# Optimization experiments

Hardware: AMD Instinct MI355X
Metric: run time of the kernel (lower is better)

Reference implementation:

```python
import jax, jax.numpy as jnp
import numpy as np

N_QUBITS = 4
B = 524288


def ry_mat(theta):
    # theta: scalar or (B,) -> (..., 2, 2) complex64
    c = jnp.cos(theta / 2).astype(jnp.complex64)
    s = jnp.sin(theta / 2).astype(jnp.complex64)
    return jnp.stack([jnp.stack([c, -s], -1), jnp.stack([s, c], -1)], -2)


def rz_mat(theta):
    e = jnp.exp(-0.5j * theta.astype(jnp.complex64))
    z = jnp.zeros_like(e)
    return jnp.stack([jnp.stack([e, z], -1), jnp.stack([z, jnp.conj(e)], -1)], -2)


def apply_shared(state, gate, wire):
    # state: (B, 2,2,2,2); gate: (2,2) shared across batch
    state = jnp.moveaxis(state, 1 + wire, -1)
    state = jnp.einsum('...a,ca->...c', state, gate)
    return jnp.moveaxis(state, -1, 1 + wire)


def apply_batched(state, gate, wire):
    # gate: (B, 2, 2), per-sample angles
    state = jnp.moveaxis(state, 1 + wire, -1)
    state = jnp.einsum('b...a,bca->b...c', state, gate)
    return jnp.moveaxis(state, -1, 1 + wire)


def cnot_01(state):
    # control wire 0 (axis 1), target wire 1 (axis 2): flip target when control=1
    return jnp.concatenate([state[:, :1], jnp.flip(state[:, 1:], axis=2)], axis=1)


def circuit(x, weights):
    # batched 4-qubit state-vector simulation; state shape (B, 2,2,2,2)
    b = x.shape[0]
    state = jnp.zeros((b,) + (2,) * N_QUBITS, jnp.complex64).at[:, 0, 0, 0, 0].set(1.0)
    # data-encoding RY layer (per-sample angles)
    for i in range(N_QUBITS):
        state = apply_batched(state, ry_mat(x[:, i]), i)
    # two repeats of (RZ, RY per wire) + CNOT(0,1); only weights[0,:,0:2] is used (faithful to source)
    for _rep in range(2):
        for i in range(N_QUBITS):
            state = apply_shared(state, rz_mat(weights[0, i, 0]), i)
            state = apply_shared(state, ry_mat(weights[0, i, 1]), i)
        state = cnot_01(state)
    probs = jnp.real(state * jnp.conj(state))  # (B,2,2,2,2)
    zexp = []
    for i in range(N_QUBITS):
        axes = tuple(a for a in range(1, 1 + N_QUBITS) if a != 1 + i)
        marg = probs.sum(axis=axes)  # (B, 2)
        zexp.append(marg[:, 0] - marg[:, 1])
    return jnp.stack(zexp, axis=-1).astype(jnp.float32)  # (B, 4)


def setup_inputs() -> dict:
    key = jax.random.key(0)
    k1, k2, k3, k4 = jax.random.split(key, 4)
    return {
        'x': jax.random.normal(k1, (B, N_QUBITS), dtype=jnp.float32),
        'weights': jax.random.normal(k2, (2, N_QUBITS, 4), dtype=jnp.float32),
        'head_w': jax.random.normal(k3, (2, N_QUBITS), dtype=jnp.float32) * 0.5,
        'head_b': jax.random.normal(k4, (2,), dtype=jnp.float32) * 0.1,
    }


def reference(x, weights, head_w, head_b):
    q = circuit(x, weights)            # (B, 4) PauliZ expectations
    return q @ head_w.T + head_b       # Linear(4, 2)
```

## Files before the change

kernel.cpp:

```cpp
#include <hip/hip_runtime.h>

#define NQ  4
#define DIM 16

__global__ __launch_bounds__(64) void prep_kernel(
    const float* __restrict__ weights,
    const float* __restrict__ head_w,
    float* __restrict__ A)
{
    __shared__ float Ure[DIM][DIM];
    __shared__ float Uim[DIM][DIM];
    const int j = threadIdx.x;
    if (j < DIM) {
        float sre[DIM], sim[DIM];
        #pragma unroll
        for (int m = 0; m < DIM; ++m) { sre[m] = (m == j) ? 1.f : 0.f; sim[m] = 0.f; }
        #pragma unroll
        for (int rep = 0; rep < 2; ++rep) {
            #pragma unroll
            for (int i = 0; i < NQ; ++i) {
                const float thz = weights[i * 4 + 0];
                const float thy = weights[i * 4 + 1];
                float sz, cz, sy, cy;
                sincosf(0.5f * thz, &sz, &cz);
                sincosf(0.5f * thy, &sy, &cy);
                const int bit = 8 >> i;
                #pragma unroll
                for (int m = 0; m < DIM; ++m) {
                    if (m & bit) continue;
                    const int m1 = m | bit;
                    const float are = sre[m],  aim = sim[m];
                    const float bre = sre[m1], bim = sim[m1];
                    const float n0re = are * cz + aim * sz;
                    const float n0im = aim * cz - are * sz;
                    const float n1re = bre * cz - bim * sz;
                    const float n1im = bim * cz + bre * sz;
                    sre[m]  = cy * n0re - sy * n1re;
                    sim[m]  = cy * n0im - sy * n1im;
                    sre[m1] = sy * n0re + cy * n1re;
                    sim[m1] = sy * n0im + cy * n1im;
                }
            }
            #pragma unroll
            for (int m = 0; m < DIM; ++m) {
                if ((m & 8) && !(m & 4)) {
                    const int m2 = m | 4;
                    const float tr = sre[m], ti = sim[m];
                    sre[m] = sre[m2]; sim[m] = sim[m2];
                    sre[m2] = tr;     sim[m2] = ti;
                }
            }
        }
        #pragma unroll
        for (int m = 0; m < DIM; ++m) { Ure[m][j] = sre[m]; Uim[m][j] = sim[m]; }
    }
    __syncthreads();

    for (int idx = threadIdx.x; idx < 2 * DIM * DIM; idx += 64) {
        const int o  = idx >> 8;
        const int jj = (idx >> 4) & 15;
        const int kk = idx & 15;
        float acc = 0.f;
        for (int m = 0; m < DIM; ++m) {
            float w = 0.f;
            #pragma unroll
            for (int i = 0; i < NQ; ++i) {
                const float hw = head_w[o * 4 + i];
                w += ((m >> (3 - i)) & 1) ? -hw : hw;
            }
            acc += w * (Ure[m][jj] * Ure[m][kk] + Uim[m][jj] * Uim[m][kk]);
        }
        A[idx] = acc;
    }
}

__global__ __launch_bounds__(256) void qmain_kernel(
    const float* __restrict__ x,
    const float* __restrict__ A,
    const float* __restrict__ head_b,
    float* __restrict__ out,
    const int Btot)
{
    __shared__ __align__(16) float sA[2 * DIM * DIM];
    __shared__ float sb[2];
    for (int i = threadIdx.x; i < 2 * DIM * DIM; i += 256) sA[i] = A[i];
    if (threadIdx.x < 2) sb[threadIdx.x] = head_b[threadIdx.x];
    __syncthreads();

    const int b = blockIdx.x * 256 + threadIdx.x;
    if (b >= Btot) return;

    const float4 xv = ((const float4*)x)[b];
    float c0, s0, c1, s1, c2, s2, c3, s3;
    __sincosf(0.5f * xv.x, &s0, &c0);
    __sincosf(0.5f * xv.y, &s1, &c1);
    __sincosf(0.5f * xv.z, &s2, &c2);
    __sincosf(0.5f * xv.w, &s3, &c3);

    float psi[DIM];
    {
        const float w0[2] = {c0, s0}, w1[2] = {c1, s1};
        const float w2[2] = {c2, s2}, w3[2] = {c3, s3};
        #pragma unroll
        for (int m = 0; m < DIM; ++m)
            psi[m] = w0[(m >> 3) & 1] * w1[(m >> 2) & 1] *
                     w2[(m >> 1) & 1] * w3[m & 1];
    }

    const float4* __restrict__ sA4 = (const float4*)sA;
    float r[2];
    #pragma unroll
    for (int o = 0; o < 2; ++o) {
        float acc = 0.f;
        #pragma unroll
        for (int jj = 0; jj < DIM; ++jj) {
            float mv = 0.f;
            #pragma unroll
            for (int kq = 0; kq < 4; ++kq) {
                const float4 a4 = sA4[(o * DIM + jj) * 4 + kq];
                mv = fmaf(a4.x, psi[kq * 4 + 0], mv);
                mv = fmaf(a4.y, psi[kq * 4 + 1], mv);
                mv = fmaf(a4.z, psi[kq * 4 + 2], mv);
                mv = fmaf(a4.w, psi[kq * 4 + 3], mv);
            }
            acc = fmaf(psi[jj], mv, acc);
        }
        r[o] = acc + sb[o];
    }
    ((float2*)out)[b] = make_float2(r[0], r[1]);
}

extern "C" void kernel_launch(void* const* d_in, const int* in_sizes, int n_in,
                              void* d_out, int out_size, void* d_ws, size_t ws_size,
                              hipStream_t stream) {
    const float* x       = (const float*)d_in[0];
    const float* weights = (const float*)d_in[1];
    const float* head_w  = (const float*)d_in[2];
    const float* head_b  = (const float*)d_in[3];
    float* out = (float*)d_out;
    float* A   = (float*)d_ws;

    const int Btot = in_sizes[0] / 4;

    prep_kernel<<<1, 64, 0, stream>>>(weights, head_w, A);
    const int blocks = (Btot + 255) / 256;
    qmain_kernel<<<blocks, 256, 0, stream>>>(x, A, head_b, out, Btot);
}
```

Measured before the change: 83.56 us.

## Rewrite quadratic form in trigonometric product basis with 81-term coefficient tensor

The per-sample quadratic form psi^T A psi is re-expressed as a contraction of a precomputed 2x81 coefficient tensor with tensor products of (1, cos x, sin x) per qubit, using double-angle identities. The main kernel now does about 27*3 FMAs per output instead of 256 and no longer stages A in shared memory or needs a block barrier. It reads the coefficients straight from global memory, where they are uniform across the wave. The head bias is folded into the tensor. A template also removes the bounds check when the batch is a multiple of 256.

Result: faster. 75.52 us (-9.6%).

```diff
diff --git a/kernel.cpp b/kernel.cpp
--- a/kernel.cpp
+++ b/kernel.cpp
@@ -6,10 +6,13 @@
 __global__ __launch_bounds__(64) void prep_kernel(
     const float* __restrict__ weights,
     const float* __restrict__ head_w,
-    float* __restrict__ A)
+    const float* __restrict__ head_b,
+    float* __restrict__ T)
 {
     __shared__ float Ure[DIM][DIM];
     __shared__ float Uim[DIM][DIM];
+    __shared__ float sA[2][DIM][DIM];
+
     const int j = threadIdx.x;
     if (j < DIM) {
         float sre[DIM], sim[DIM];
@@ -70,64 +73,77 @@
             }
             acc += w * (Ure[m][jj] * Ure[m][kk] + Uim[m][jj] * Uim[m][kk]);
         }
-        A[idx] = acc;
+        sA[o][jj][kk] = acc;
+    }
+    __syncthreads();
+
+    for (int idx = threadIdx.x; idx < 2 * 81; idx += 64) {
+        const int o  = idx / 81;
+        const int r  = idx % 81;
+        const int a0 = r / 27, a1 = (r / 9) % 3, a2 = (r / 3) % 3, a3 = r % 3;
+        const int xm = ((a0 == 2) << 3) | ((a1 == 2) << 2) | ((a2 == 2) << 1) | (a3 == 2);
+        const int sm = ((a0 == 1) << 3) | ((a1 == 1) << 2) | ((a2 == 1) << 1) | (a3 == 1);
+        float acc = 0.f;
+        #pragma unroll
+        for (int jj = 0; jj < DIM; ++jj) {
+            const float s = (__popc(jj & sm) & 1) ? -1.f : 1.f;
+            acc += s * sA[o][jj][jj ^ xm];
+        }
+        float t = acc * 0.0625f;
+        if (r == 0) t += head_b[o];
+        T[idx] = t;
     }
 }
 
+template <bool CHK>
 __global__ __launch_bounds__(256) void qmain_kernel(
-    const float* __restrict__ x,
-    const float* __restrict__ A,
-    const float* __restrict__ head_b,
-    float* __restrict__ out,
+    const float4* __restrict__ x4,
+    const float* __restrict__ T,
+    float2* __restrict__ out,
     const int Btot)
 {
-    __shared__ __align__(16) float sA[2 * DIM * DIM];
-    __shared__ float sb[2];
-    for (int i = threadIdx.x; i < 2 * DIM * DIM; i += 256) sA[i] = A[i];
-    if (threadIdx.x < 2) sb[threadIdx.x] = head_b[threadIdx.x];
-    __syncthreads();
+    const int b = blockIdx.x * 256 + threadIdx.x;
+    if (CHK && b >= Btot) return;
 
-    const int b = blockIdx.x * 256 + threadIdx.x;
-    if (b >= Btot) return;
+    const float4 xv = x4[b];
+    float c0, s0, c1, s1, c2, s2, c3, s3;
+    __sincosf(xv.x, &s0, &c0);
+    __sincosf(xv.y, &s1, &c1);
+    __sincosf(xv.z, &s2, &c2);
+    __sincosf(xv.w, &s3, &c3);
 
-    const float4 xv = ((const float4*)x)[b];
-    float c0, s0, c1, s1, c2, s2, c3, s3;
-    __sincosf(0.5f * xv.x, &s0, &c0);
-    __sincosf(0.5f * xv.y, &s1, &c1);
-    __sincosf(0.5f * xv.z, &s2, &c2);
-    __sincosf(0.5f * xv.w, &s3, &c3);
+    const float v0[3] = {1.f, c0, s0};
+    const float v1[3] = {1.f, c1, s1};
+    const float v2[3] = {1.f, c2, s2};
+    const float v3[3] = {1.f, c3, s3};
 
-    float psi[DIM];
-    {
-        const float w0[2] = {c0, s0}, w1[2] = {c1, s1};
-        const float w2[2] = {c2, s2}, w3[2] = {c3, s3};
+    float u[27];
+    #pragma unroll
+    for (int a = 0; a < 3; ++a) {
         #pragma unroll
-        for (int m = 0; m < DIM; ++m)
-            psi[m] = w0[(m >> 3) & 1] * w1[(m >> 2) & 1] *
-                     w2[(m >> 1) & 1] * w3[m & 1];
+        for (int bq = 0; bq < 3; ++bq) {
+            const float vv = v1[a] * v2[bq];
+            #pragma unroll
+            for (int cq = 0; cq < 3; ++cq)
+                u[a * 9 + bq * 3 + cq] = vv * v3[cq];
+        }
     }
 
-    const float4* __restrict__ sA4 = (const float4*)sA;
     float r[2];
     #pragma unroll
     for (int o = 0; o < 2; ++o) {
         float acc = 0.f;
         #pragma unroll
-        for (int jj = 0; jj < DIM; ++jj) {
-            float mv = 0.f;
+        for (int a0 = 0; a0 < 3; ++a0) {
+            float d = 0.f;
             #pragma unroll
-            for (int kq = 0; kq < 4; ++kq) {
-                const float4 a4 = sA4[(o * DIM + jj) * 4 + kq];
-                mv = fmaf(a4.x, psi[kq * 4 + 0], mv);
-                mv = fmaf(a4.y, psi[kq * 4 + 1], mv);
-                mv = fmaf(a4.z, psi[kq * 4 + 2], mv);
-                mv = fmaf(a4.w, psi[kq * 4 + 3], mv);
-            }
-            acc = fmaf(psi[jj], mv, acc);
+            for (int jj = 0; jj < 27; ++jj)
+                d = fmaf(T[o * 81 + a0 * 27 + jj], u[jj], d);
+            acc = fmaf(v0[a0], d, acc);
         }
-        r[o] = acc + sb[o];
+        r[o] = acc;
     }
-    ((float2*)out)[b] = make_float2(r[0], r[1]);
+    out[b] = make_float2(r[0], r[1]);
 }
 
 extern "C" void kernel_launch(void* const* d_in, const int* in_sizes, int n_in,
@@ -138,11 +154,17 @@
     const float* head_w  = (const float*)d_in[2];
     const float* head_b  = (const float*)d_in[3];
     float* out = (float*)d_out;
-    float* A   = (float*)d_ws;
+    float* T   = (float*)d_ws;
 
     const int Btot = in_sizes[0] / 4;
 
-    prep_kernel<<<1, 64, 0, stream>>>(weights, head_w, A);
-    const int blocks = (Btot + 255) / 256;
-    qmain_kernel<<<blocks, 256, 0, stream>>>(x, A, head_b, out, Btot);
+    prep_kernel<<<1, 64, 0, stream>>>(weights, head_w, head_b, T);
+
+    if ((Btot & 255) == 0) {
+        qmain_kernel<false><<<Btot / 256, 256, 0, stream>>>(
+            (const float4*)x, T, (float2*)out, Btot);
+    } else {
+        qmain_kernel<true><<<(Btot + 255) / 256, 256, 0, stream>>>(
+            (const float4*)x, T, (float2*)out, Btot);
+    }
 }
```
